# Kernel optimization log

Measured on AMD Instinct MI355X. Metric: run time of the kernel, lower is better.

Reference implementation:

```python
import jax, jax.numpy as jnp
import numpy as np

B, T, C = 4, 2048, 768
N_HEAD = 12
HS = C // N_HEAD

def setup_inputs() -> dict:
    key = jax.random.key(0)
    ks = jax.random.split(key, 5)
    s = 0.02
    return {
        "x": jax.random.normal(ks[0], (B, T, C), dtype=jnp.float32),
        "w_attn": jax.random.normal(ks[1], (C, 3 * C), dtype=jnp.float32) * s,
        "b_attn": jnp.zeros((3 * C,), dtype=jnp.float32),
        "w_proj": jax.random.normal(ks[2], (C, C), dtype=jnp.float32) * s,
        "b_proj": jnp.zeros((C,), dtype=jnp.float32),
    }

def reference(x, w_attn, b_attn, w_proj, b_proj):
    Bx, Tx, Cx = x.shape
    qkv = x @ w_attn + b_attn                      # [B,T,3C]
    q, k, v = jnp.split(qkv, 3, axis=-1)
    # [B,H,T,hs]
    q = q.reshape(Bx, Tx, N_HEAD, HS).transpose(0, 2, 1, 3)
    k = k.reshape(Bx, Tx, N_HEAD, HS).transpose(0, 2, 1, 3)
    v = v.reshape(Bx, Tx, N_HEAD, HS).transpose(0, 2, 1, 3)
    att = jnp.einsum('bhqd,bhkd->bhqk', q, k) * (1.0 / jnp.sqrt(jnp.float32(HS)))
    mask = jnp.tril(jnp.ones((Tx, Tx), dtype=bool))  # causal
    att = jnp.where(mask, att, jnp.float32(-jnp.inf))
    att = jax.nn.softmax(att, axis=-1)
    y = jnp.einsum('bhqk,bhkd->bhqd', att, v)
    y = y.transpose(0, 2, 1, 3).reshape(Bx, Tx, Cx)
    return y @ w_proj + b_proj
```

## Files before the change

kernel.cpp:

```cpp
#include <hip/hip_runtime.h>

#define BB 4
#define TT 2048
#define CC 768
#define QKVW 2304
#define NHH 12
#define HSS 64
#define NQT64 (TT / 64)

typedef __attribute__((ext_vector_type(4))) float floatx4;
typedef __attribute__((ext_vector_type(8))) short shortx8;
typedef __attribute__((ext_vector_type(4))) short shortx4;

__device__ __forceinline__ unsigned short f2bf(float f) {
  union { float f; unsigned int u; } cv; cv.f = f;
  unsigned int u = cv.u;
  u += 0x7FFFu + ((u >> 16) & 1u);
  return (unsigned short)(u >> 16);
}
__device__ __forceinline__ unsigned short bfp(float f) {
  union { float f; unsigned int u; } cv; cv.f = f;
  return (unsigned short)((cv.u + 0x8000u) >> 16);
}
__device__ __forceinline__ unsigned short bft(float f) {
  union { float f; unsigned int u; } cv; cv.f = f;
  return (unsigned short)(cv.u >> 16);
}

__device__ __forceinline__ void async_copy16(const void* g, void* l) {
  __builtin_amdgcn_global_load_lds(
      (const __attribute__((address_space(1))) unsigned int*)g,
      (__attribute__((address_space(3))) unsigned int*)l, 16, 0, 0);
}

__global__ void convert_x(const float* __restrict__ x, unsigned short* __restrict__ xb, int n4) {
  int i = blockIdx.x * blockDim.x + threadIdx.x;
  const int stride = gridDim.x * blockDim.x;
  for (; i < n4; i += stride) {
    float4 v = ((const float4*)x)[i];
    shortx4 s;
    s.x = (short)f2bf(v.x); s.y = (short)f2bf(v.y);
    s.z = (short)f2bf(v.z); s.w = (short)f2bf(v.w);
    ((shortx4*)xb)[i] = s;
  }
}

__global__ __launch_bounds__(256)
void transpose_w(const float* __restrict__ w, unsigned short* __restrict__ wt, int K, int N) {
  __shared__ short tile[64 * 68];
  const int n0 = blockIdx.x * 64, k0 = blockIdx.y * 64;
  const int tid = threadIdx.x;
  {
    const int tr = tid >> 4, tc = (tid & 15) * 4;
#pragma unroll
    for (int i = 0; i < 4; ++i) {
      float4 v = *(const float4*)(w + (size_t)(k0 + tr + 16 * i) * N + n0 + tc);
      short* d = &tile[(tr + 16 * i) * 68 + tc];
      d[0] = (short)f2bf(v.x); d[1] = (short)f2bf(v.y);
      d[2] = (short)f2bf(v.z); d[3] = (short)f2bf(v.w);
    }
  }
  __syncthreads();
  {
    const int wr = tid >> 3, wc = (tid & 7) * 8;
#pragma unroll
    for (int j = 0; j < 2; ++j) {
      const int n = wr + 32 * j;
      shortx8 s;
#pragma unroll
      for (int e = 0; e < 8; ++e) s[e] = tile[(wc + e) * 68 + n];
      *(shortx8*)(wt + (size_t)(n0 + n) * K + k0 + wc) = s;
    }
  }
}

__global__ __launch_bounds__(256)
void transpose_v(const unsigned short* __restrict__ qkv, unsigned short* __restrict__ Vt) {
  __shared__ short tile[64 * 72];
  const int t0 = blockIdx.x * 64;
  const int bh = blockIdx.y;
  const int b = bh / NHH, h = bh % NHH;
  const int tid = threadIdx.x;
  {
    const int tr = tid >> 3, tc = (tid & 7) * 8;
#pragma unroll
    for (int i = 0; i < 2; ++i) {
      shortx8 v = *(const shortx8*)(qkv + ((size_t)(b * TT + t0 + tr + 32 * i)) * QKVW + 2 * CC + h * HSS + tc);
      *(shortx8*)&tile[(tr + 32 * i) * 72 + tc] = v;
    }
  }
  __syncthreads();
  {
    const int dr = tid >> 3, tc = (tid & 7) * 8;
    const int base = (tc & 32) + ((tc >> 3) & 3) * 4;
#pragma unroll
    for (int j = 0; j < 2; ++j) {
      const int d = dr + 32 * j;
      shortx8 s;
#pragma unroll
      for (int e = 0; e < 8; ++e)
        s[e] = tile[(base + (e >> 2) * 16 + (e & 3)) * 72 + d];
      *(shortx8*)(Vt + ((size_t)bh * HSS + d) * TT + t0 + tc) = s;
    }
  }
}

template<bool OUT_BF16, bool QSCALE>
__global__ __launch_bounds__(256)
void gemm_tn(const unsigned short* __restrict__ A, const unsigned short* __restrict__ Bt,
             const float* __restrict__ bias, void* __restrict__ Cp, int M, int N, int K) {
  __shared__ short As[3][128 * 32];
  __shared__ short Bs[3][128 * 32];
  const int tid = threadIdx.x, lane = tid & 63, wave = tid >> 6;
  const int row = lane & 15, quad = lane >> 4;
  const int wm = (wave >> 1) * 64, wn = (wave & 1) * 64;
  const int m0 = blockIdx.x * 128, n0 = blockIdx.y * 128;

  floatx4 acc[4][4] = {};

  const int lr = lane >> 2;
  const int csrc = (lane & 3) ^ ((lr >> 1) & 3);
  const int sr = wave * 32 + lr;
  const unsigned short* aP = A + (size_t)(m0 + sr) * K + csrc * 8;
  const unsigned short* bP = Bt + (size_t)(n0 + sr) * K + csrc * 8;
  const int sOff = (wave * 32) * 32;

  const int qsw = (quad ^ ((row >> 1) & 3)) * 8;

  const int nk = K >> 5;

  auto stage = [&](int t, int bi) {
#pragma unroll
    for (int i = 0; i < 2; ++i) {
      async_copy16(aP + (size_t)(16 * i) * K + t * 32, &As[bi][sOff + i * 512]);
      async_copy16(bP + (size_t)(16 * i) * K + t * 32, &Bs[bi][sOff + i * 512]);
    }
  };

  stage(0, 0);
  if (nk > 1) stage(1, 1);
  int cb = 0;
  for (int t = 0; t < nk; ++t) {
    int pb = cb + 2; if (pb >= 3) pb -= 3;
    if (t + 2 < nk) {
      stage(t + 2, pb);
      asm volatile("s_waitcnt vmcnt(8)" ::: "memory");
    } else if (t + 1 < nk) {
      asm volatile("s_waitcnt vmcnt(4)" ::: "memory");
    } else {
      asm volatile("s_waitcnt vmcnt(0)" ::: "memory");
    }
    __builtin_amdgcn_sched_barrier(0);
    __builtin_amdgcn_s_barrier();
    __builtin_amdgcn_sched_barrier(0);
    {
      shortx8 af[4], bf[4];
#pragma unroll
      for (int g = 0; g < 4; ++g) {
        af[g] = *(const shortx8*)&As[cb][(wm + g * 16 + row) * 32 + qsw];
        bf[g] = *(const shortx8*)&Bs[cb][(wn + g * 16 + row) * 32 + qsw];
      }
#pragma unroll
      for (int mg = 0; mg < 4; ++mg)
#pragma unroll
        for (int ng = 0; ng < 4; ++ng)
          acc[mg][ng] = __builtin_amdgcn_mfma_f32_16x16x32_bf16(af[mg], bf[ng], acc[mg][ng], 0, 0, 0);
    }
    __builtin_amdgcn_sched_barrier(0);
    __builtin_amdgcn_s_barrier();
    __builtin_amdgcn_sched_barrier(0);
    cb = (cb + 1 == 3) ? 0 : cb + 1;
  }

#pragma unroll
  for (int mg = 0; mg < 4; ++mg) {
    const int m = m0 + wm + mg * 16 + quad * 4;
#pragma unroll
    for (int ng = 0; ng < 4; ++ng) {
      const int n = n0 + wn + ng * 16 + row;
      const float bv = bias[n];
      const float scl = (QSCALE && n < CC) ? 0.180336881f : 1.0f;
#pragma unroll
      for (int r = 0; r < 4; ++r) {
        const float val = (acc[mg][ng][r] + bv) * scl;
        if (OUT_BF16) ((unsigned short*)Cp)[(size_t)(m + r) * N + n] = f2bf(val);
        else          ((float*)Cp)[(size_t)(m + r) * N + n] = val;
      }
    }
  }
}

__global__ __launch_bounds__(256)
void attn_kernel(const unsigned short* __restrict__ qkv, const unsigned short* __restrict__ Vt,
                 unsigned short* __restrict__ y) {
  __shared__ short Ksh[3][64 * 64];
  __shared__ short Vsh[3][64 * 64];

  const int id = blockIdx.x;
  const int xcd = id & 7;
  const int slot = id >> 3;
  const int qt = NQT64 - 1 - slot / 6;
  const int gl = slot % 6;
  const int g = xcd * 6 + gl;
  const int h = g % NHH, b = g / NHH;
  const int bh = b * NHH + h;
  const int tid = threadIdx.x, lane = tid & 63, wave = tid >> 6;
  const int row = lane & 15, quad = lane >> 4;
  const int qhalf = wave & 1;
  const int khalf = wave >> 1;

  const unsigned short* kSrc = qkv + ((size_t)(b * TT)) * QKVW + CC + h * HSS;
  const unsigned short* vSrc = Vt + ((size_t)bh * HSS) * TT;

  const shortx8 ones8 = {(short)0x3F80, (short)0x3F80, (short)0x3F80, (short)0x3F80,
                         (short)0x3F80, (short)0x3F80, (short)0x3F80, (short)0x3F80};

  const int qb0 = qt * 64 + qhalf * 32;
  const int nk = qt + 1;

  const int lr8 = lane >> 3;
  const int csw = ((lane & 7) ^ lr8) * 8;
  size_t kOff[2], vOff[2];
#pragma unroll
  for (int i = 0; i < 2; ++i) {
    const int r = wave * 16 + i * 8 + lr8;
    kOff[i] = (size_t)r * QKVW + csw;
    vOff[i] = (size_t)r * TT + csw;
  }
  const int sBase = (wave * 16) * 64;

  const int r7 = row & 7;
  int kR[2][2], vR[4];
#pragma unroll
  for (int mg = 0; mg < 2; ++mg) {
    const int krow = khalf * 32 + mg * 16 + row;
    kR[mg][0] = krow * 64 + ((quad ^ r7) * 8);
    kR[mg][1] = krow * 64 + (((quad + 4) ^ r7) * 8);
  }
#pragma unroll
  for (int dg = 0; dg < 4; ++dg)
    vR[dg] = (dg * 16 + row) * 64 + (((khalf * 4 + quad) ^ r7) * 8);

  shortx8 qf[2][2];
#pragma unroll
  for (int qg = 0; qg < 2; ++qg) {
    const unsigned short* qp = qkv + ((size_t)(b * TT) + qb0 + qg * 16 + row) * QKVW + h * HSS;
    qf[qg][0] = *(const shortx8*)(qp + quad * 8);
    qf[qg][1] = *(const shortx8*)(qp + 32 + quad * 8);
  }
  asm volatile("s_waitcnt vmcnt(0)" ::: "memory");

  floatx4 lf[2] = {(floatx4)(0.0f), (floatx4)(0.0f)};
  floatx4 o[2][4];
#pragma unroll
  for (int qg = 0; qg < 2; ++qg)
#pragma unroll
    for (int dg = 0; dg < 4; ++dg) o[qg][dg] = (floatx4)(0.0f);

  auto stage = [&](int t, int bi) {
#pragma unroll
    for (int i = 0; i < 2; ++i) {
      async_copy16(kSrc + (size_t)(t * 64) * QKVW + kOff[i], &Ksh[bi][sBase + i * 512]);
      async_copy16(vSrc + (size_t)(t * 64) + vOff[i],        &Vsh[bi][sBase + i * 512]);
    }
  };

  stage(0, 0);
  if (nk > 1) stage(1, 1);
  int cb = 0;
  for (int kt = 0; kt < nk; ++kt) {
    int pb = cb + 2; if (pb >= 3) pb -= 3;
    if (kt + 2 < nk) {
      stage(kt + 2, pb);
      asm volatile("s_waitcnt vmcnt(8)" ::: "memory");
    } else if (kt + 1 < nk) {
      asm volatile("s_waitcnt vmcnt(4)" ::: "memory");
    } else {
      asm volatile("s_waitcnt vmcnt(0)" ::: "memory");
    }
    __builtin_amdgcn_sched_barrier(0);
    __builtin_amdgcn_s_barrier();
    __builtin_amdgcn_sched_barrier(0);
    {
      const short* Kc = &Ksh[cb][0];
      const short* Vc = &Vsh[cb][0];
      __builtin_amdgcn_s_setprio(1);
      shortx4 pfr[2][2];
#pragma unroll
      for (int mg = 0; mg < 2; ++mg) {
        const shortx8 kf0 = *(const shortx8*)&Kc[kR[mg][0]];
        const shortx8 kf1 = *(const shortx8*)&Kc[kR[mg][1]];
#pragma unroll
        for (int qg = 0; qg < 2; ++qg) {
          floatx4 t = __builtin_amdgcn_mfma_f32_16x16x32_bf16(kf0, qf[qg][0], (floatx4)(0.0f), 0, 0, 0);
          t = __builtin_amdgcn_mfma_f32_16x16x32_bf16(kf1, qf[qg][1], t, 0, 0, 0);
          if (kt == qt) {
            const int kg = kt * 64 + khalf * 32 + mg * 16 + quad * 4;
            const int qv = qb0 + qg * 16 + row;
#pragma unroll
            for (int r = 0; r < 4; ++r)
              if (kg + r > qv) t[r] = -1e30f;
          }
          shortx4 pk;
#pragma unroll
          for (int r = 0; r < 4; ++r) pk[r] = (short)bft(__builtin_amdgcn_exp2f(t[r]));
          pfr[qg][mg] = pk;
        }
      }
      shortx8 pk8[2];
#pragma unroll
      for (int qg = 0; qg < 2; ++qg) {
        pk8[qg] = __builtin_shufflevector(pfr[qg][0], pfr[qg][1], 0, 1, 2, 3, 4, 5, 6, 7);
        lf[qg] = __builtin_amdgcn_mfma_f32_16x16x32_bf16(pk8[qg], ones8, lf[qg], 0, 0, 0);
      }
#pragma unroll
      for (int dg = 0; dg < 4; ++dg) {
        const shortx8 vf = *(const shortx8*)&Vc[vR[dg]];
#pragma unroll
        for (int qg = 0; qg < 2; ++qg)
          o[qg][dg] = __builtin_amdgcn_mfma_f32_16x16x32_bf16(pk8[qg], vf, o[qg][dg], 0, 0, 0);
      }
      __builtin_amdgcn_s_setprio(0);
    }
    __builtin_amdgcn_sched_barrier(0);
    __builtin_amdgcn_s_barrier();
    __builtin_amdgcn_sched_barrier(0);
    cb = (cb + 1 == 3) ? 0 : cb + 1;
  }

  floatx4* red4 = (floatx4*)(&Ksh[0][0]);
  const int rbase = (qhalf * 64 + lane) * 11;
  if (khalf) {
#pragma unroll
    for (int qg = 0; qg < 2; ++qg) {
#pragma unroll
      for (int dg = 0; dg < 4; ++dg) red4[rbase + qg * 4 + dg] = o[qg][dg];
      red4[rbase + 8 + qg] = lf[qg];
    }
  }
  __syncthreads();
  if (!khalf) {
#pragma unroll
    for (int qg = 0; qg < 2; ++qg) {
#pragma unroll
      for (int dg = 0; dg < 4; ++dg) o[qg][dg] += red4[rbase + qg * 4 + dg];
      lf[qg] += red4[rbase + 8 + qg];
    }
#pragma unroll
    for (int qg = 0; qg < 2; ++qg) {
#pragma unroll
      for (int r = 0; r < 4; ++r) {
        const float lo = 1.0f / lf[qg][r];
        unsigned short* yp = y + ((size_t)(b * TT) + qb0 + qg * 16 + quad * 4 + r) * CC + h * HSS;
#pragma unroll
        for (int dg = 0; dg < 4; ++dg)
          yp[dg * 16 + row] = bfp(o[qg][dg][r] * lo);
      }
    }
  }
}

extern "C" void kernel_launch(void* const* d_in, const int* in_sizes, int n_in,
                              void* d_out, int out_size, void* d_ws, size_t ws_size,
                              hipStream_t stream) {
  const float* x      = (const float*)d_in[0];
  const float* w_attn = (const float*)d_in[1];
  const float* b_attn = (const float*)d_in[2];
  const float* w_proj = (const float*)d_in[3];
  const float* b_proj = (const float*)d_in[4];
  float* out = (float*)d_out;

  char* ws = (char*)d_ws;
  unsigned short* xb  = (unsigned short*)ws;
  unsigned short* y   = (unsigned short*)ws;
  unsigned short* qkv = (unsigned short*)(ws + 12582912);
  unsigned short* wta = (unsigned short*)(ws + 50331648);
  unsigned short* Vt  = (unsigned short*)(ws + 50331648);
  unsigned short* wtp = (unsigned short*)(ws + 62914560);

  const int M = BB * TT;

  convert_x<<<1024, 256, 0, stream>>>(x, xb, (M * CC) / 4);
  transpose_w<<<dim3(QKVW / 64, CC / 64), 256, 0, stream>>>(w_attn, wta, CC, QKVW);
  transpose_w<<<dim3(CC / 64, CC / 64), 256, 0, stream>>>(w_proj, wtp, CC, CC);

  gemm_tn<true, true><<<dim3(M / 128, QKVW / 128), 256, 0, stream>>>(
      xb, wta, b_attn, (void*)qkv, M, QKVW, CC);

  transpose_v<<<dim3(TT / 64, BB * NHH), 256, 0, stream>>>(qkv, Vt);

  attn_kernel<<<dim3(NQT64 * NHH * BB), 256, 0, stream>>>(qkv, Vt, y);

  gemm_tn<false, false><<<dim3(M / 128, CC / 128), 256, 0, stream>>>(
      y, wtp, b_proj, (void*)out, M, CC, CC);
}
```

Baseline: 204.1 us.

## Fuse prep kernels and write transposed V directly from QKV GEMM epilogue

Merges the x conversion and both weight transposes into one launch with a block-id dispatch, which cuts two kernel launches. The QKV GEMM epilogue now writes the V columns straight into the permuted Vt layout, so the separate transpose_v pass and its global memory round trip are dropped when the workspace is large enough. In exchange the epilogue does scattered 8-byte stores into Vt, and the workspace layout moves Vt and wtp to new offsets.

```diff
diff --git a/kernel.cpp b/kernel.cpp
--- a/kernel.cpp
+++ b/kernel.cpp
@@ -33,23 +33,34 @@
       (__attribute__((address_space(3))) unsigned int*)l, 16, 0, 0);
 }
 
-__global__ void convert_x(const float* __restrict__ x, unsigned short* __restrict__ xb, int n4) {
-  int i = blockIdx.x * blockDim.x + threadIdx.x;
-  const int stride = gridDim.x * blockDim.x;
-  for (; i < n4; i += stride) {
-    float4 v = ((const float4*)x)[i];
-    shortx4 s;
-    s.x = (short)f2bf(v.x); s.y = (short)f2bf(v.y);
-    s.z = (short)f2bf(v.z); s.w = (short)f2bf(v.w);
-    ((shortx4*)xb)[i] = s;
-  }
-}
-
 __global__ __launch_bounds__(256)
-void transpose_w(const float* __restrict__ w, unsigned short* __restrict__ wt, int K, int N) {
+void prep_fused(const float* __restrict__ x, unsigned short* __restrict__ xb, int n4,
+                const float* __restrict__ wa, unsigned short* __restrict__ wta,
+                const float* __restrict__ wp, unsigned short* __restrict__ wtp) {
   __shared__ short tile[64 * 68];
-  const int n0 = blockIdx.x * 64, k0 = blockIdx.y * 64;
+  const int bid = blockIdx.x;
   const int tid = threadIdx.x;
+  if (bid < 1024) {
+    int i = bid * 256 + tid;
+    const int stride = 1024 * 256;
+    for (; i < n4; i += stride) {
+      float4 v = ((const float4*)x)[i];
+      shortx4 s;
+      s.x = (short)f2bf(v.x); s.y = (short)f2bf(v.y);
+      s.z = (short)f2bf(v.z); s.w = (short)f2bf(v.w);
+      ((shortx4*)xb)[i] = s;
+    }
+    return;
+  }
+  const float* w; unsigned short* wt; int N, n0, k0;
+  if (bid < 1456) {
+    const int t = bid - 1024;
+    w = wa; wt = wta; N = QKVW; n0 = (t % 36) * 64; k0 = (t / 36) * 64;
+  } else {
+    const int t = bid - 1456;
+    w = wp; wt = wtp; N = CC;   n0 = (t % 12) * 64; k0 = (t / 12) * 64;
+  }
+  const int K = CC;
   {
     const int tr = tid >> 4, tc = (tid & 15) * 4;
 #pragma unroll
@@ -105,10 +116,11 @@
   }
 }
 
-template<bool OUT_BF16, bool QSCALE>
+template<bool OUT_BF16, bool QSCALE, bool VSTORE>
 __global__ __launch_bounds__(256)
 void gemm_tn(const unsigned short* __restrict__ A, const unsigned short* __restrict__ Bt,
-             const float* __restrict__ bias, void* __restrict__ Cp, int M, int N, int K) {
+             const float* __restrict__ bias, void* __restrict__ Cp,
+             unsigned short* __restrict__ VtOut, int M, int N, int K) {
   __shared__ short As[3][128 * 32];
   __shared__ short Bs[3][128 * 32];
   const int tid = threadIdx.x, lane = tid & 63, wave = tid >> 6;
@@ -172,6 +184,26 @@
     cb = (cb + 1 == 3) ? 0 : cb + 1;
   }
 
+  if (VSTORE && n0 >= 2 * CC) {
+    const int bb = m0 >> 11;
+#pragma unroll
+    for (int mg = 0; mg < 4; ++mg) {
+      const int tb = (m0 & 2047) + wm + mg * 16 + quad * 4;
+      const int t_store = (tb & ~31) | ((tb & 12) << 1) | ((tb >> 2) & 4);
+#pragma unroll
+      for (int ng = 0; ng < 4; ++ng) {
+        const int n = n0 + wn + ng * 16 + row;
+        const float bv = bias[n];
+        const int f = n - 2 * CC;
+        shortx4 pk;
+#pragma unroll
+        for (int r = 0; r < 4; ++r) pk[r] = (short)f2bf(acc[mg][ng][r] + bv);
+        *(shortx4*)(VtOut + ((size_t)(bb * NHH + (f >> 6)) * HSS + (f & 63)) * TT + t_store) = pk;
+      }
+    }
+    return;
+  }
+
 #pragma unroll
   for (int mg = 0; mg < 4; ++mg) {
     const int m = m0 + wm + mg * 16 + quad * 4;
@@ -371,26 +403,32 @@
   float* out = (float*)d_out;
 
   char* ws = (char*)d_ws;
+  const int M = BB * TT;
+  const size_t vtBytes = (size_t)BB * NHH * HSS * TT * 2;
+
   unsigned short* xb  = (unsigned short*)ws;
   unsigned short* y   = (unsigned short*)ws;
   unsigned short* qkv = (unsigned short*)(ws + 12582912);
   unsigned short* wta = (unsigned short*)(ws + 50331648);
-  unsigned short* Vt  = (unsigned short*)(ws + 50331648);
-  unsigned short* wtp = (unsigned short*)(ws + 62914560);
-
-  const int M = BB * TT;
-
-  convert_x<<<1024, 256, 0, stream>>>(x, xb, (M * CC) / 4);
-  transpose_w<<<dim3(QKVW / 64, CC / 64), 256, 0, stream>>>(w_attn, wta, CC, QKVW);
-  transpose_w<<<dim3(CC / 64, CC / 64), 256, 0, stream>>>(w_proj, wtp, CC, CC);
-
-  gemm_tn<true, true><<<dim3(M / 128, QKVW / 128), 256, 0, stream>>>(
-      xb, wta, b_attn, (void*)qkv, M, QKVW, CC);
-
-  transpose_v<<<dim3(TT / 64, BB * NHH), 256, 0, stream>>>(qkv, Vt);
+
+  const bool fusedV = ws_size >= (size_t)53870592 + vtBytes + 1179648;
+  unsigned short* Vt  = (unsigned short*)(ws + (fusedV ? (size_t)53870592 : (size_t)50331648));
+  unsigned short* wtp = (unsigned short*)(ws + (fusedV ? (size_t)53870592 + vtBytes
+                                                       : (size_t)62914560));
+
+  prep_fused<<<1600, 256, 0, stream>>>(x, xb, (M * CC) / 4, w_attn, wta, w_proj, wtp);
+
+  if (fusedV) {
+    gemm_tn<true, true, true><<<dim3(M / 128, QKVW / 128), 256, 0, stream>>>(
+        xb, wta, b_attn, (void*)qkv, Vt, M, QKVW, CC);
+  } else {
+    gemm_tn<true, true, false><<<dim3(M / 128, QKVW / 128), 256, 0, stream>>>(
+        xb, wta, b_attn, (void*)qkv, nullptr, M, QKVW, CC);
+    transpose_v<<<dim3(TT / 64, BB * NHH), 256, 0, stream>>>(qkv, Vt);
+  }
 
   attn_kernel<<<dim3(NQT64 * NHH * BB), 256, 0, stream>>>(qkv, Vt, y);
 
-  gemm_tn<false, false><<<dim3(M / 128, CC / 128), 256, 0, stream>>>(
-      y, wtp, b_proj, (void*)out, M, CC, CC);
-}
+  gemm_tn<false, false, false><<<dim3(M / 128, CC / 128), 256, 0, stream>>>(
+      y, wtp, b_proj, (void*)out, nullptr, M, CC, CC);
+}
```

Result: no change. 203.6 us (-0.2%).
